# Kernel optimization log

Measured on AMD Instinct MI355X. Metric: run time of the kernel, lower is better.

## Reference

```python
import jax, jax.numpy as jnp
import numpy as np

IN_F, H, T, NUM_CLASSES, WINDOW_HALF = 14, 24, 25, 4, 12


def _lstm_dir(x_tbf, w_ih, w_hh, b_ih, b_hh, reverse):
    # x_tbf: [T,B,F]; w_ih: [4H,F]; w_hh: [4H,H]; biases: [4H]
    B = x_tbf.shape[1]
    xw = jnp.einsum('tbf,gf->tbg', x_tbf, w_ih) + b_ih + b_hh  # [T,B,4H]

    def step(carry, xw_t):
        h, c = carry
        gates = xw_t + h @ w_hh.T
        i, f, g, o = jnp.split(gates, 4, axis=-1)
        i, f, o = jax.nn.sigmoid(i), jax.nn.sigmoid(f), jax.nn.sigmoid(o)
        g = jnp.tanh(g)
        c = f * c + i * g
        h = o * jnp.tanh(c)
        return (h, c), h

    h0 = jnp.zeros((B, H), x_tbf.dtype)
    c0 = jnp.zeros((B, H), x_tbf.dtype)
    _, hs = jax.lax.scan(step, (h0, c0), xw, reverse=reverse)
    return hs  # [T,B,H], in original time order


def setup_inputs() -> dict:
    key = jax.random.key(0)
    ks = jax.random.split(key, 12)
    s_ih = 1.0 / np.sqrt(H)
    u = lambda k, shape: jax.random.uniform(k, shape, jnp.float32, -s_ih, s_ih)
    return {
        'x': jax.random.normal(ks[0], (65536, T, IN_F), jnp.float32),
        'w_ih_f': u(ks[1], (4 * H, IN_F)),
        'w_hh_f': u(ks[2], (4 * H, H)),
        'b_ih_f': u(ks[3], (4 * H,)),
        'b_hh_f': u(ks[4], (4 * H,)),
        'w_ih_b': u(ks[5], (4 * H, IN_F)),
        'w_hh_b': u(ks[6], (4 * H, H)),
        'b_ih_b': u(ks[7], (4 * H,)),
        'b_hh_b': u(ks[8], (4 * H,)),
        'head_w': u(ks[9], (NUM_CLASSES, 2 * H)),
        'head_b': u(ks[10], (NUM_CLASSES,)),
    }


def reference(x, w_ih_f, w_hh_f, b_ih_f, b_hh_f, w_ih_b, w_hh_b, b_ih_b, b_hh_b, head_w, head_b):
    x_tbf = jnp.transpose(x, (1, 0, 2))  # [T,B,F]
    h_f = _lstm_dir(x_tbf, w_ih_f, w_hh_f, b_ih_f, b_hh_f, reverse=False)
    h_b = _lstm_dir(x_tbf, w_ih_b, w_hh_b, b_ih_b, b_hh_b, reverse=True)
    center = jnp.concatenate([h_f[WINDOW_HALF], h_b[WINDOW_HALF]], axis=-1)  # [B,2H]
    # dropout is identity in eval mode
    return center @ head_w.T + head_b  # [B,4]
```

## Files before the change

kernel.cpp:

```cpp
#include <hip/hip_runtime.h>

typedef __attribute__((ext_vector_type(8))) short frag8;
typedef __attribute__((ext_vector_type(4))) float f4;
typedef __attribute__((ext_vector_type(4), aligned(8))) float f4a;
typedef __attribute__((ext_vector_type(4))) unsigned int u4;
typedef __attribute__((ext_vector_type(2))) unsigned int u2;
typedef __attribute__((ext_vector_type(2))) float f2;

namespace {
constexpr int T_STEPS = 25;
constexpr int IN_F    = 14;
constexpr int H       = 24;
constexpr int NSTEP   = 13;
constexpr int STEP_B  = 512;
constexpr int WAVE_REGION = 14 * STEP_B;
constexpr float LOG2E    = 1.4426950408889634f;
constexpr float TWOLOG2E = 2.8853900817779268f;
}

#if __has_builtin(__builtin_amdgcn_exp2f)
#define EXP2F(v) __builtin_amdgcn_exp2f(v)
#else
#define EXP2F(v) __expf(0.6931471805599453f * (v))
#endif

__device__ __forceinline__ unsigned short bf16_rne(float f) {
    unsigned int u = __float_as_uint(f);
    u += 0x7fff + ((u >> 16) & 1);
    return (unsigned short)(u >> 16);
}
__device__ __forceinline__ float bf16_to_f(unsigned short s) {
    return __uint_as_float(((unsigned int)s) << 16);
}
__device__ __forceinline__ float fast_rcp(float x) { return __builtin_amdgcn_rcpf(x); }

__device__ __forceinline__ f2 pk_add(f2 a, f2 b) {
    f2 d; asm("v_pk_add_f32 %0, %1, %2" : "=v"(d) : "v"(a), "v"(b)); return d;
}
__device__ __forceinline__ f2 pk_mul(f2 a, f2 b) {
    f2 d; asm("v_pk_mul_f32 %0, %1, %2" : "=v"(d) : "v"(a), "v"(b)); return d;
}
__device__ __forceinline__ f2 pk_fma(f2 a, f2 b, f2 c) {
    f2 d; asm("v_pk_fma_f32 %0, %1, %2, %3" : "=v"(d) : "v"(a), "v"(b), "v"(c)); return d;
}

__global__ void pack_mfma(const float* __restrict__ wif, const float* __restrict__ whf,
                          const float* __restrict__ bif, const float* __restrict__ bhf,
                          const float* __restrict__ wib, const float* __restrict__ whb,
                          const float* __restrict__ bib, const float* __restrict__ bhb,
                          unsigned short* __restrict__ ws)
{
    const int gid = blockIdx.x * 256 + threadIdx.x;
    if (gid >= 1536) return;
    const int lane = gid & 63;
    const int tile = (gid >> 6) % 6;
    const int m    = (gid / 384) & 1;
    const int dir  = gid / 768;
    const int rm = lane & 15, qA = lane >> 4;
    int g, u_row;
    if (tile < 4) { g = tile; u_row = rm; }
    else {
        const int r = rm & 3, qq = rm >> 2;
        g = (tile == 4 ? 0 : 2) + (r >> 1);
        u_row = ((r & 1) ? 20 : 16) + qq;
    }
    const float* Wx = dir ? wib : wif;
    const float* Wh = dir ? whb : whf;
    const float* bi = dir ? bib : bif;
    const float* bh = dir ? bhb : bhf;
    const int rowW = g * 24 + u_row;
    const float scale = (g == 2) ? TWOLOG2E : -LOG2E;
    unsigned short vals[8];
    #pragma unroll
    for (int j = 0; j < 8; ++j) {
        unsigned short o;
        if (j < 6) {
            const int uh = (j < 4) ? (qA * 4 + j) : ((j == 4 ? 16 : 20) + qA);
            o = bf16_rne(scale * Wh[rowW * H + uh]);
        } else {
            const int jj = j - 6;
            if (m == 0) {
                o = bf16_rne(scale * Wx[rowW * IN_F + 4 * qA + jj]);
            } else if (qA < 3) {
                o = bf16_rne(scale * Wx[rowW * IN_F + 4 * qA + 2 + jj]);
            } else {
                const float b = scale * (bi[rowW] + bh[rowW]);
                const unsigned short hi = bf16_rne(b);
                o = (jj == 0) ? hi : bf16_rne(b - bf16_to_f(hi));
            }
        }
        vals[j] = o;
    }
    unsigned short* d = ws + (size_t)gid * 8;
    #pragma unroll
    for (int j = 0; j < 8; ++j) d[j] = vals[j];
}

__device__ __forceinline__ void gates_pair(float ai0, float ai1, float af0, float af1,
                                           float ag0, float ag1, float ao0, float ao1,
                                           f2& cvs, f2& Hp,
                                           f2 ONE, f2 NEGONE, f2 T2L, f2 NT2L)
{
    f2 ei, ef, eg, eo;
    ei.x = EXP2F(ai0); ei.y = EXP2F(ai1);
    ef.x = EXP2F(af0); ef.y = EXP2F(af1);
    eg.x = EXP2F(ag0); eg.y = EXP2F(ag1);
    eo.x = EXP2F(ao0); eo.y = EXP2F(ao1);
    const f2 efp1 = pk_add(ef, ONE);
    const f2 P    = pk_mul(pk_add(ei, ONE), pk_add(eg, ONE));
    const f2 Df   = pk_mul(P, efp1);
    const float r = fast_rcp(Df.x * Df.y);
    f2 Rf; Rf.x = r * Df.y; Rf.y = r * Df.x;
    const f2 X = pk_mul(pk_fma(eg, T2L, NT2L), efp1);
    cvs = pk_mul(pk_fma(cvs, P, X), Rf);
    f2 ec; ec.x = EXP2F(cvs.x); ec.y = EXP2F(cvs.y);
    const f2 Do = pk_mul(pk_add(eo, ONE), pk_add(ec, ONE));
    const float r2 = fast_rcp(Do.x * Do.y);
    f2 Ro; Ro.x = r2 * Do.y; Ro.y = r2 * Do.x;
    Hp = pk_mul(pk_add(ec, NEGONE), Ro);
}

__device__ __forceinline__ unsigned int perm_hi16(float a_hi, float a_lo) {
    return __builtin_amdgcn_perm(__float_as_uint(a_hi), __float_as_uint(a_lo), 0x07060302u);
}

__global__ __launch_bounds__(128, 4)
void bilstm_mfma(const float* __restrict__ x, const unsigned short* __restrict__ wpk,
                 const float* __restrict__ head_w, const float* __restrict__ head_b,
                 float* __restrict__ out, int B)
{
    __align__(16) __shared__ unsigned char arena[2 * WAVE_REGION];

    const int tid  = threadIdx.x;
    const int wave = __builtin_amdgcn_readfirstlane(tid >> 6);
    const int lane = tid & 63;
    const int q    = lane >> 4;
    const int col  = lane & 15;
    const int b0   = blockIdx.x * 16;

    frag8 Aw[2][6];
    #pragma unroll
    for (int m = 0; m < 2; ++m)
        #pragma unroll
        for (int t = 0; t < 6; ++t)
            Aw[m][t] = ((const frag8*)wpk)[((wave * 2 + m) * 6 + t) * 64 + lane];

    unsigned char* xbase = arena + wave * WAVE_REGION;

    {
        const int c  = lane & 3;
        const int e  = lane >> 2;
        const bool c3 = (c == 3);
        const int ldo = c3 ? 40 : c * 16;
        const int woff = (c * 16 + e) * 8;
        #pragma unroll 4
        for (int t = 0; t < NSTEP; ++t) {
            const int tt = wave ? (T_STEPS - 1 - t) : t;
            const char* xr = (const char*)x
                           + ((size_t)(b0 + e) * T_STEPS + tt) * (IN_F * 4) + ldo;
            const f4a v = *(const f4a*)xr;
            unsigned int p0, p1;
            asm("v_cvt_pk_bf16_f32 %0, %1, %2" : "=v"(p0) : "v"(v.x), "v"(v.y));
            asm("v_cvt_pk_bf16_f32 %0, %1, %2" : "=v"(p1) : "v"(v.z), "v"(v.w));
            const unsigned int wa = c3 ? p1 : p0;
            const unsigned int wb = c3 ? 0x3F803F80u : p1;
            *(u2*)(xbase + t * STEP_B + woff) = (u2){wa, wb};
        }
    }

    const int xoff = lane * 8;

    const f2 ONE    = {1.0f, 1.0f};
    const f2 NEGONE = {-1.0f, -1.0f};
    const f2 T2L    = {TWOLOG2E, TWOLOG2E};
    const f2 NT2L   = {-TWOLOG2E, -TWOLOG2E};

    f2 cvl = {0.f, 0.f}, cvh = {0.f, 0.f}, cvs = {0.f, 0.f};
    f2 Hlo, Hhi, Hs;
    unsigned int uh0 = 0, uh1 = 0, uh2 = 0;
    unsigned int ul0 = 0, ul1 = 0, ul2 = 0;
    const f4 zc = {0.f, 0.f, 0.f, 0.f};

    u2 xw = *(const u2*)(xbase + xoff);

    #pragma unroll 1
    for (int s = 0; s < NSTEP; ++s) {
        const u2 xn = *(const u2*)(xbase + (s + 1) * STEP_B + xoff);
        const frag8 B0 = __builtin_bit_cast(frag8, (u4){uh0, uh1, uh2, xw.x});
        const frag8 B1 = __builtin_bit_cast(frag8, (u4){ul0, ul1, ul2, xw.y});
        f4 acc[6];
        #pragma unroll
        for (int t = 0; t < 6; ++t) {
            acc[t] = __builtin_amdgcn_mfma_f32_16x16x32_bf16(Aw[0][t], B0, zc,     0, 0, 0);
            acc[t] = __builtin_amdgcn_mfma_f32_16x16x32_bf16(Aw[1][t], B1, acc[t], 0, 0, 0);
        }
        gates_pair(acc[0][0], acc[0][1], acc[1][0], acc[1][1],
                   acc[2][0], acc[2][1], acc[3][0], acc[3][1],
                   cvl, Hlo, ONE, NEGONE, T2L, NT2L);
        gates_pair(acc[0][2], acc[0][3], acc[1][2], acc[1][3],
                   acc[2][2], acc[2][3], acc[3][2], acc[3][3],
                   cvh, Hhi, ONE, NEGONE, T2L, NT2L);
        gates_pair(acc[4][0], acc[4][1], acc[4][2], acc[4][3],
                   acc[5][0], acc[5][1], acc[5][2], acc[5][3],
                   cvs, Hs, ONE, NEGONE, T2L, NT2L);

        f2 Tl, Th, Ts;
        Tl.x = __uint_as_float(__float_as_uint(Hlo.x) & 0xFFFF0000u);
        Tl.y = __uint_as_float(__float_as_uint(Hlo.y) & 0xFFFF0000u);
        Th.x = __uint_as_float(__float_as_uint(Hhi.x) & 0xFFFF0000u);
        Th.y = __uint_as_float(__float_as_uint(Hhi.y) & 0xFFFF0000u);
        Ts.x = __uint_as_float(__float_as_uint(Hs.x) & 0xFFFF0000u);
        Ts.y = __uint_as_float(__float_as_uint(Hs.y) & 0xFFFF0000u);
        const f2 Ll = pk_fma(Tl, NEGONE, Hlo);
        const f2 Lh = pk_fma(Th, NEGONE, Hhi);
        const f2 Ls = pk_fma(Ts, NEGONE, Hs);
        uh0 = perm_hi16(Hlo.y, Hlo.x); uh1 = perm_hi16(Hhi.y, Hhi.x);
        uh2 = perm_hi16(Hs.y, Hs.x);
        ul0 = perm_hi16(Ll.y, Ll.x);   ul1 = perm_hi16(Lh.y, Lh.x);
        ul2 = perm_hi16(Ls.y, Ls.x);

        xw = xn;
    }

    *(f2*)(xbase + col * 96 + q * 16)     = Hlo;
    *(f2*)(xbase + col * 96 + q * 16 + 8) = Hhi;
    *(float*)(xbase + col * 96 + 64 + q * 4) = Hs.x;
    *(float*)(xbase + col * 96 + 80 + q * 4) = Hs.y;

    __syncthreads();

    if (tid < 64) {
        const int e = tid >> 2, cls = tid & 3;
        float acc = head_b[cls];
        const float* hf = (const float*)(arena + e * 96);
        const float* hb = (const float*)(arena + WAVE_REGION + e * 96);
        #pragma unroll
        for (int u = 0; u < H; ++u)
            acc += hf[u] * head_w[cls * 2 * H + u] + hb[u] * head_w[cls * 2 * H + H + u];
        out[(size_t)b0 * 4 + tid] = acc;
    }
}

extern "C" void kernel_launch(void* const* d_in, const int* in_sizes, int n_in,
                              void* d_out, int out_size, void* d_ws, size_t ws_size,
                              hipStream_t stream)
{
    const float* x      = (const float*)d_in[0];
    const float* w_ih_f = (const float*)d_in[1];
    const float* w_hh_f = (const float*)d_in[2];
    const float* b_ih_f = (const float*)d_in[3];
    const float* b_hh_f = (const float*)d_in[4];
    const float* w_ih_b = (const float*)d_in[5];
    const float* w_hh_b = (const float*)d_in[6];
    const float* b_ih_b = (const float*)d_in[7];
    const float* b_hh_b = (const float*)d_in[8];
    const float* head_w = (const float*)d_in[9];
    const float* head_b = (const float*)d_in[10];
    float* out = (float*)d_out;
    unsigned short* ws = (unsigned short*)d_ws;

    const int B = in_sizes[0] / (T_STEPS * IN_F);

    hipLaunchKernelGGL(pack_mfma, dim3(6), dim3(256), 0, stream,
                       w_ih_f, w_hh_f, b_ih_f, b_hh_f,
                       w_ih_b, w_hh_b, b_ih_b, b_hh_b, ws);
    hipLaunchKernelGGL(bilstm_mfma, dim3((B + 15) / 16), dim3(128), 0, stream,
                       x, ws, head_w, head_b, out, B);
}
```

Baseline: 165.9 us.

## Pack two batch groups per 256-thread block and batch x loads up front

Each block now runs two 16-sample groups (four waves) instead of one, which halves the grid size and doubles the LDS arena per block. The x staging loop now issues all 13 loads into registers before converting and storing them, rather than interleaving a load and a store each step. The aim is to cut per-block launch overhead and expose more memory-level parallelism in the input load. The trade-off is higher register pressure from holding 13 vectors and a larger LDS footprint, which may reduce occupancy under launch_bounds(256,4).

After: 165.7 us. About the same (-0.1%).

```diff
diff --git a/kernel.cpp b/kernel.cpp
--- a/kernel.cpp
+++ b/kernel.cpp
@@ -124,19 +124,23 @@
     return __builtin_amdgcn_perm(__float_as_uint(a_hi), __float_as_uint(a_lo), 0x07060302u);
 }
 
-__global__ __launch_bounds__(128, 4)
+__global__ __launch_bounds__(256, 4)
 void bilstm_mfma(const float* __restrict__ x, const unsigned short* __restrict__ wpk,
                  const float* __restrict__ head_w, const float* __restrict__ head_b,
                  float* __restrict__ out, int B)
 {
-    __align__(16) __shared__ unsigned char arena[2 * WAVE_REGION];
+    __align__(16) __shared__ unsigned char arena[4 * WAVE_REGION];
 
     const int tid  = threadIdx.x;
-    const int wave = __builtin_amdgcn_readfirstlane(tid >> 6);
+    const int pr   = __builtin_amdgcn_readfirstlane(tid >> 7);
+    const int wave = __builtin_amdgcn_readfirstlane((tid >> 6) & 1);
     const int lane = tid & 63;
     const int q    = lane >> 4;
     const int col  = lane & 15;
-    const int b0   = blockIdx.x * 16;
+    const int nG   = (B + 15) / 16;
+    int g = blockIdx.x * 2 + pr;
+    if (g >= nG) g = nG - 1;
+    const int b0   = g * 16;
 
     frag8 Aw[2][6];
     #pragma unroll
@@ -145,7 +149,7 @@
         for (int t = 0; t < 6; ++t)
             Aw[m][t] = ((const frag8*)wpk)[((wave * 2 + m) * 6 + t) * 64 + lane];
 
-    unsigned char* xbase = arena + wave * WAVE_REGION;
+    unsigned char* xbase = arena + (pr * 2 + wave) * WAVE_REGION;
 
     {
         const int c  = lane & 3;
@@ -153,15 +157,19 @@
         const bool c3 = (c == 3);
         const int ldo = c3 ? 40 : c * 16;
         const int woff = (c * 16 + e) * 8;
-        #pragma unroll 4
+        const int dstep = wave ? -(IN_F * 4) : (IN_F * 4);
+        const char* xcol = (const char*)x
+                         + ((size_t)(b0 + e) * T_STEPS + (wave ? T_STEPS - 1 : 0))
+                           * (IN_F * 4) + ldo;
+        f4a v[NSTEP];
+        #pragma unroll
+        for (int t = 0; t < NSTEP; ++t)
+            v[t] = *(const f4a*)(xcol + t * dstep);
+        #pragma unroll
         for (int t = 0; t < NSTEP; ++t) {
-            const int tt = wave ? (T_STEPS - 1 - t) : t;
-            const char* xr = (const char*)x
-                           + ((size_t)(b0 + e) * T_STEPS + tt) * (IN_F * 4) + ldo;
-            const f4a v = *(const f4a*)xr;
             unsigned int p0, p1;
-            asm("v_cvt_pk_bf16_f32 %0, %1, %2" : "=v"(p0) : "v"(v.x), "v"(v.y));
-            asm("v_cvt_pk_bf16_f32 %0, %1, %2" : "=v"(p1) : "v"(v.z), "v"(v.w));
+            asm("v_cvt_pk_bf16_f32 %0, %1, %2" : "=v"(p0) : "v"(v[t].x), "v"(v[t].y));
+            asm("v_cvt_pk_bf16_f32 %0, %1, %2" : "=v"(p1) : "v"(v[t].z), "v"(v[t].w));
             const unsigned int wa = c3 ? p1 : p0;
             const unsigned int wb = c3 ? 0x3F803F80u : p1;
             *(u2*)(xbase + t * STEP_B + woff) = (u2){wa, wb};
@@ -229,15 +237,19 @@
 
     __syncthreads();
 
-    if (tid < 64) {
-        const int e = tid >> 2, cls = tid & 3;
+    if (tid < 128) {
+        const int pr2 = tid >> 6;
+        const int e = (tid & 63) >> 2, cls = tid & 3;
+        int g2 = blockIdx.x * 2 + pr2;
+        if (g2 >= nG) g2 = nG - 1;
+        const unsigned char* region = arena + pr2 * 2 * WAVE_REGION;
         float acc = head_b[cls];
-        const float* hf = (const float*)(arena + e * 96);
-        const float* hb = (const float*)(arena + WAVE_REGION + e * 96);
+        const float* hf = (const float*)(region + e * 96);
+        const float* hb = (const float*)(region + WAVE_REGION + e * 96);
         #pragma unroll
         for (int u = 0; u < H; ++u)
             acc += hf[u] * head_w[cls * 2 * H + u] + hb[u] * head_w[cls * 2 * H + H + u];
-        out[(size_t)b0 * 4 + tid] = acc;
+        out[(size_t)g2 * 64 + (tid & 63)] = acc;
     }
 }
 
@@ -260,10 +272,12 @@
     unsigned short* ws = (unsigned short*)d_ws;
 
     const int B = in_sizes[0] / (T_STEPS * IN_F);
+    const int nG = (B + 15) / 16;
+    const int nBlk = (nG + 1) / 2;
 
     hipLaunchKernelGGL(pack_mfma, dim3(6), dim3(256), 0, stream,
                        w_ih_f, w_hh_f, b_ih_f, b_hh_f,
                        w_ih_b, w_hh_b, b_ih_b, b_hh_b, ws);
-    hipLaunchKernelGGL(bilstm_mfma, dim3((B + 15) / 16), dim3(128), 0, stream,
+    hipLaunchKernelGGL(bilstm_mfma, dim3(nBlk), dim3(256), 0, stream,
                        x, ws, head_w, head_b, out, B);
 }
```
